# Kernel optimization log

Measured on AMD Instinct MI355X. Metric: run time of the kernel, lower is better.

## Reference

```python
import jax, jax.numpy as jnp
import numpy as np

B, N, D = 256, 512, 64  # batch, positions, channels; units = spatial_units = D


def setup_inputs() -> dict:
    key = jax.random.key(0)
    ks = jax.random.split(key, 9)
    g = 1.0 / np.sqrt(D)  # glorot-ish scale for square matrices
    return {
        "x": jax.random.normal(ks[0], (B, N, D), dtype=jnp.float32),
        "Wq_t": jax.random.normal(ks[1], (D, D), dtype=jnp.float32) * g,
        "Wk_t": jax.random.normal(ks[2], (D, D), dtype=jnp.float32) * g,
        "Wv_t": jax.random.normal(ks[3], (D, D), dtype=jnp.float32) * g,
        "Wq_s": jax.random.normal(ks[4], (D, D), dtype=jnp.float32) * g,
        "Wk_s": jax.random.normal(ks[5], (D, D), dtype=jnp.float32) * g,
        "Wv_s": jax.random.normal(ks[6], (D, D), dtype=jnp.float32) * g,
        "Wd_t": jax.random.normal(ks[7], (D, D), dtype=jnp.float32) * g,
        "bd_t": jnp.zeros((D,), dtype=jnp.float32),
        "Wd_s": jax.random.normal(ks[8], (D, D), dtype=jnp.float32) * g,
        "bd_s": jnp.zeros((D,), dtype=jnp.float32),
    }


def _branch(x, Wq, Wk, Wv, Wd, bd):
    # x: [B, N, D]; one self-attention branch followed by a Dense layer.
    q = jnp.einsum("bnd,de->bne", x, Wq)
    k = jnp.einsum("bnd,de->bne", x, Wk)
    v = jnp.einsum("bnd,de->bne", x, Wv)
    scale = 1.0 / jnp.sqrt(jnp.asarray(Wk.shape[-1], dtype=x.dtype))
    scores = jnp.einsum("bne,bme->bnm", q, k) * scale  # [B, N, N]
    w = jax.nn.softmax(scores, axis=-1)
    attn = jnp.einsum("bnm,bmd->bnd", w, v)
    return jnp.einsum("bnd,de->bne", attn, Wd) + bd


def reference(x, Wq_t, Wk_t, Wv_t, Wq_s, Wk_s, Wv_s, Wd_t, bd_t, Wd_s, bd_s):
    temporal = _branch(x, Wq_t, Wk_t, Wv_t, Wd_t, bd_t)
    spatial = _branch(x, Wq_s, Wk_s, Wv_s, Wd_s, bd_s)
    gate = jax.nn.sigmoid(temporal + spatial)
    return x * gate
```

## Files before the change

kernel.cpp:

```cpp
#include <hip/hip_runtime.h>

typedef __attribute__((ext_vector_type(8))) short short8;
typedef __attribute__((ext_vector_type(4))) short short4v;
typedef __attribute__((ext_vector_type(4))) float float4v;

#define MFMA16(a, b, c) __builtin_amdgcn_mfma_f32_16x16x32_bf16((a), (b), (c), 0, 0, 0)

constexpr int kN = 512;
constexpr int kD = 64;
constexpr int kThreads = 512;

constexpr int LDS_TOTAL_BYTES = 163840;

static __device__ __forceinline__ unsigned short f2bf(float f) {
  unsigned int u = __float_as_uint(f);
  u = (u + 0x7fffu + ((u >> 16) & 1u)) >> 16;
  return (unsigned short)u;
}

__global__ __launch_bounds__(kThreads, 2) void ts_attn_fused(
    const float* __restrict__ x, const float* __restrict__ Wq_t,
    const float* __restrict__ Wk_t, const float* __restrict__ Wv_t,
    const float* __restrict__ Wq_s, const float* __restrict__ Wk_s,
    const float* __restrict__ Wv_s, const float* __restrict__ Wd_t,
    const float* __restrict__ bd_t, const float* __restrict__ Wd_s,
    const float* __restrict__ bd_s, float* __restrict__ out,
    unsigned short* __restrict__ qws) {
  extern __shared__ __align__(16) unsigned short smem_us[];
  unsigned short* Ksw = smem_us;
  unsigned short* Vsw = smem_us + 32768;
  unsigned short* Wdsw = smem_us + 65536;
  unsigned short* Rreg = smem_us + 69632;

  const int tid = threadIdx.x;
  const int wv = tid >> 6;
  const int lane = tid & 63;
  const int ln = lane & 15;
  const int quad = lane >> 4;
  const int b = blockIdx.x;

  const float* xb = x + (size_t)b * (kN * kD);
  float* outb = out + (size_t)b * (kN * kD);
  unsigned short* qb = qws + (size_t)b * (kN * kD);

  float bdsum[4];
#pragma unroll
  for (int nt = 0; nt < 4; ++nt) bdsum[nt] = bd_t[nt * 16 + ln] + bd_s[nt * 16 + ln];

#pragma unroll 1
  for (int br = 0; br < 2; ++br) {
    const float* Wq = br ? Wq_s : Wq_t;
    const float* Wk = br ? Wk_s : Wk_t;
    const float* Wv = br ? Wv_s : Wv_t;
    const float* Wd = br ? Wd_s : Wd_t;

    {
      const int d = tid >> 3;
      const int e0 = (tid & 7) * 8;
      const int base = (d >> 3) * 512 + (d & 7);
      const float* srcs[4] = {Wq, Wk, Wv, Wd};
      unsigned short* dsts[4] = {Rreg, Rreg + 4096, Rreg + 8192, Wdsw};
#pragma unroll
      for (int g = 0; g < 4; ++g) {
        const float4v* p = reinterpret_cast<const float4v*>(srcs[g] + d * 64 + e0);
        const float4v u = p[0];
        const float4v v = p[1];
        unsigned short* dst = dsts[g];
#pragma unroll
        for (int i = 0; i < 4; ++i) dst[base + (e0 + i) * 8] = f2bf(u[i]);
#pragma unroll
        for (int i = 0; i < 4; ++i) dst[base + (e0 + 4 + i) * 8] = f2bf(v[i]);
      }
    }
    __syncthreads();

#pragma unroll 1
    for (int mi = 0; mi < 4; ++mi) {
      const int mt = wv + mi * 8;
      const int mrow = mt * 16 + ln;
      short8 xa0, xa1;
      {
        const float4v* p0 = reinterpret_cast<const float4v*>(xb + mrow * 64 + quad * 8);
        const float4v u0 = p0[0], v0 = p0[1];
        const float4v* p1 = reinterpret_cast<const float4v*>(xb + mrow * 64 + 32 + quad * 8);
        const float4v u1 = p1[0], v1 = p1[1];
#pragma unroll
        for (int i = 0; i < 4; ++i) {
          xa0[i] = (short)f2bf(u0[i]);
          xa0[4 + i] = (short)f2bf(v0[i]);
          xa1[i] = (short)f2bf(u1[i]);
          xa1[4 + i] = (short)f2bf(v1[i]);
        }
      }
#pragma unroll
      for (int g = 0; g < 3; ++g) {
        const unsigned short* Wl = Rreg + g * 4096;
#pragma unroll
        for (int nt = 0; nt < 4; ++nt) {
          const short8 b0 = *reinterpret_cast<const short8*>(Wl + quad * 512 + (nt * 16 + ln) * 8);
          const short8 b1 = *reinterpret_cast<const short8*>(Wl + (4 + quad) * 512 + (nt * 16 + ln) * 8);
          float4v acc = {0.f, 0.f, 0.f, 0.f};
          acc = MFMA16(xa0, b0, acc);
          acc = MFMA16(xa1, b1, acc);
          if (g == 0) {
            const int ehi = nt * 2 + (ln >> 3);
            const int elo = ln & 7;
#pragma unroll
            for (int r = 0; r < 4; ++r)
              qb[ehi * 4096 + (mt * 16 + quad * 4 + r) * 8 + elo] = f2bf(acc[r]);
          } else if (g == 1) {
            const int ehi = nt * 2 + (ln >> 3);
            const int elo = ln & 7;
#pragma unroll
            for (int r = 0; r < 4; ++r)
              Ksw[ehi * 4096 + (mt * 16 + quad * 4 + r) * 8 + elo] = f2bf(acc[r]);
          } else {
            short4v pk;
#pragma unroll
            for (int r = 0; r < 4; ++r) pk[r] = (short)f2bf(acc[r]);
            const int vbase =
                (mt * 2 + (quad >> 1)) * 512 + (nt * 16 + ln) * 8 + (quad & 1) * 4;
            *reinterpret_cast<short4v*>(Vsw + vbase) = pk;
          }
        }
      }
    }
    __syncthreads();

    unsigned short* buf = Rreg + wv * 1152;
#pragma unroll 1
    for (int qi = 0; qi < 4; ++qi) {
      const int qt = wv + qi * 8;
      const short8 q0 = *reinterpret_cast<const short8*>(qb + quad * 4096 + (qt * 16 + ln) * 8);
      const short8 q1 = *reinterpret_cast<const short8*>(qb + (4 + quad) * 4096 + (qt * 16 + ln) * 8);

      float4v s[32];
#pragma unroll
      for (int nt = 0; nt < 32; ++nt) {
        const short8 k0 = *reinterpret_cast<const short8*>(Ksw + quad * 4096 + (nt * 16 + ln) * 8);
        const short8 k1 = *reinterpret_cast<const short8*>(Ksw + (4 + quad) * 4096 + (nt * 16 + ln) * 8);
        float4v acc = {0.f, 0.f, 0.f, 0.f};
        acc = MFMA16(q0, k0, acc);
        acc = MFMA16(q1, k1, acc);
        s[nt] = acc;
      }

      float mx[4] = {-3.0e38f, -3.0e38f, -3.0e38f, -3.0e38f};
#pragma unroll
      for (int nt = 0; nt < 32; ++nt)
#pragma unroll
        for (int r = 0; r < 4; ++r) mx[r] = fmaxf(mx[r], s[nt][r]);
#pragma unroll
      for (int dd = 1; dd < 16; dd <<= 1)
#pragma unroll
        for (int r = 0; r < 4; ++r) mx[r] = fmaxf(mx[r], __shfl_xor(mx[r], dd, 64));

      float sum[4] = {0.f, 0.f, 0.f, 0.f};
      float4v o[4];
#pragma unroll
      for (int i = 0; i < 4; ++i) o[i] = (float4v){0.f, 0.f, 0.f, 0.f};

#pragma unroll
      for (int kc = 0; kc < 16; ++kc) {
#pragma unroll
        for (int t2 = 0; t2 < 2; ++t2) {
          const int nt = kc * 2 + t2;
#pragma unroll
          for (int r = 0; r < 4; ++r) {
            const float p = __expf((s[nt][r] - mx[r]) * 0.125f);
            sum[r] += p;
            buf[(quad * 4 + r) * 72 + t2 * 16 + ln] = f2bf(p);
          }
        }
        asm volatile("s_waitcnt lgkmcnt(0)" ::: "memory");
        const short8 pa = *reinterpret_cast<const short8*>(buf + ln * 72 + quad * 8);
#pragma unroll
        for (int nto = 0; nto < 4; ++nto) {
          const short8 vf =
              *reinterpret_cast<const short8*>(Vsw + (kc * 4 + quad) * 512 + (nto * 16 + ln) * 8);
          o[nto] = MFMA16(pa, vf, o[nto]);
        }
      }

#pragma unroll
      for (int dd = 1; dd < 16; dd <<= 1)
#pragma unroll
        for (int r = 0; r < 4; ++r) sum[r] += __shfl_xor(sum[r], dd, 64);
      float inv[4];
#pragma unroll
      for (int r = 0; r < 4; ++r) inv[r] = 1.0f / sum[r];

#pragma unroll
      for (int nto = 0; nto < 4; ++nto)
#pragma unroll
        for (int r = 0; r < 4; ++r)
          buf[(quad * 4 + r) * 72 + nto * 16 + ln] = f2bf(o[nto][r] * inv[r]);
      asm volatile("s_waitcnt lgkmcnt(0)" ::: "memory");
      const short8 a0 = *reinterpret_cast<const short8*>(buf + ln * 72 + quad * 8);
      const short8 a1 = *reinterpret_cast<const short8*>(buf + ln * 72 + 32 + quad * 8);

#pragma unroll
      for (int nt = 0; nt < 4; ++nt) {
        const short8 w0 = *reinterpret_cast<const short8*>(Wdsw + quad * 512 + (nt * 16 + ln) * 8);
        const short8 w1 = *reinterpret_cast<const short8*>(Wdsw + (4 + quad) * 512 + (nt * 16 + ln) * 8);
        float4v d4 = {0.f, 0.f, 0.f, 0.f};
        d4 = MFMA16(a0, w0, d4);
        d4 = MFMA16(a1, w1, d4);
        const int m0 = qt * 16 + quad * 4;
        const int col = nt * 16 + ln;
        if (br == 0) {
#pragma unroll
          for (int r = 0; r < 4; ++r) outb[(m0 + r) * 64 + col] = d4[r];
        } else {
#pragma unroll
          for (int r = 0; r < 4; ++r) {
            const float z = outb[(m0 + r) * 64 + col] + d4[r] + bdsum[nt];
            const float gate = 1.0f / (1.0f + __expf(-z));
            outb[(m0 + r) * 64 + col] = xb[(m0 + r) * 64 + col] * gate;
          }
        }
      }
    }
    __syncthreads();
  }
}

extern "C" void kernel_launch(void* const* d_in, const int* in_sizes, int n_in,
                              void* d_out, int out_size, void* d_ws, size_t ws_size,
                              hipStream_t stream) {
  const float* x = (const float*)d_in[0];
  const float* Wq_t = (const float*)d_in[1];
  const float* Wk_t = (const float*)d_in[2];
  const float* Wv_t = (const float*)d_in[3];
  const float* Wq_s = (const float*)d_in[4];
  const float* Wk_s = (const float*)d_in[5];
  const float* Wv_s = (const float*)d_in[6];
  const float* Wd_t = (const float*)d_in[7];
  const float* bd_t = (const float*)d_in[8];
  const float* Wd_s = (const float*)d_in[9];
  const float* bd_s = (const float*)d_in[10];
  float* out = (float*)d_out;
  unsigned short* qws = (unsigned short*)d_ws;

  hipFuncSetAttribute(reinterpret_cast<const void*>(ts_attn_fused),
                      hipFuncAttributeMaxDynamicSharedMemorySize, LDS_TOTAL_BYTES);
  ts_attn_fused<<<dim3(256), dim3(kThreads), LDS_TOTAL_BYTES, stream>>>(
      x, Wq_t, Wk_t, Wv_t, Wq_s, Wk_s, Wv_s, Wd_t, bd_t, Wd_s, bd_s, out, qws);
}
```

Before: 193.4 us.

## Stream QK scores without max pass, double threads, keep temporal branch in registers

```diff
diff --git a/kernel.cpp b/kernel.cpp
--- a/kernel.cpp
+++ b/kernel.cpp
@@ -8,9 +8,9 @@
 
 constexpr int kN = 512;
 constexpr int kD = 64;
-constexpr int kThreads = 512;
-
-constexpr int LDS_TOTAL_BYTES = 163840;
+constexpr int kThreads = 1024;
+
+constexpr int LDS_TOTAL_BYTES = 79872 * 2;
 
 static __device__ __forceinline__ unsigned short f2bf(float f) {
   unsigned int u = __float_as_uint(f);
@@ -18,7 +18,7 @@
   return (unsigned short)u;
 }
 
-__global__ __launch_bounds__(kThreads, 2) void ts_attn_fused(
+__global__ __launch_bounds__(kThreads, 4) void ts_attn_fused(
     const float* __restrict__ x, const float* __restrict__ Wq_t,
     const float* __restrict__ Wk_t, const float* __restrict__ Wv_t,
     const float* __restrict__ Wq_s, const float* __restrict__ Wk_s,
@@ -30,7 +30,7 @@
   unsigned short* Ksw = smem_us;
   unsigned short* Vsw = smem_us + 32768;
   unsigned short* Wdsw = smem_us + 65536;
-  unsigned short* Rreg = smem_us + 69632;
+  unsigned short* rep = smem_us + 69632;
 
   const int tid = threadIdx.x;
   const int wv = tid >> 6;
@@ -43,9 +43,15 @@
   float* outb = out + (size_t)b * (kN * kD);
   unsigned short* qb = qws + (size_t)b * (kN * kD);
 
+  const int sd = tid >> 4;
+  const int se0 = (tid & 15) * 4;
+  const int sbase = (sd >> 3) * 512 + (sd & 7);
+
   float bdsum[4];
 #pragma unroll
   for (int nt = 0; nt < 4; ++nt) bdsum[nt] = bd_t[nt * 16 + ln] + bd_s[nt * 16 + ln];
+
+  float4v acc_t[2][4];
 
 #pragma unroll 1
   for (int br = 0; br < 2; ++br) {
@@ -55,28 +61,21 @@
     const float* Wd = br ? Wd_s : Wd_t;
 
     {
-      const int d = tid >> 3;
-      const int e0 = (tid & 7) * 8;
-      const int base = (d >> 3) * 512 + (d & 7);
-      const float* srcs[4] = {Wq, Wk, Wv, Wd};
-      unsigned short* dsts[4] = {Rreg, Rreg + 4096, Rreg + 8192, Wdsw};
-#pragma unroll
-      for (int g = 0; g < 4; ++g) {
-        const float4v* p = reinterpret_cast<const float4v*>(srcs[g] + d * 64 + e0);
-        const float4v u = p[0];
-        const float4v v = p[1];
+      const float* srcs[3] = {Wq, Wk, Wv};
+      unsigned short* dsts[3] = {rep, rep + 4096, Wdsw};
+#pragma unroll
+      for (int g = 0; g < 3; ++g) {
+        const float4v u = *reinterpret_cast<const float4v*>(srcs[g] + sd * 64 + se0);
         unsigned short* dst = dsts[g];
 #pragma unroll
-        for (int i = 0; i < 4; ++i) dst[base + (e0 + i) * 8] = f2bf(u[i]);
-#pragma unroll
-        for (int i = 0; i < 4; ++i) dst[base + (e0 + 4 + i) * 8] = f2bf(v[i]);
+        for (int i = 0; i < 4; ++i) dst[sbase + (se0 + i) * 8] = f2bf(u[i]);
       }
     }
     __syncthreads();
 
 #pragma unroll 1
-    for (int mi = 0; mi < 4; ++mi) {
-      const int mt = wv + mi * 8;
+    for (int mi = 0; mi < 2; ++mi) {
+      const int mt = wv + mi * 16;
       const int mrow = mt * 16 + ln;
       short8 xa0, xa1;
       {
@@ -94,7 +93,7 @@
       }
 #pragma unroll
       for (int g = 0; g < 3; ++g) {
-        const unsigned short* Wl = Rreg + g * 4096;
+        const unsigned short* Wl = (g == 0) ? rep : (g == 1) ? (rep + 4096) : Wdsw;
 #pragma unroll
         for (int nt = 0; nt < 4; ++nt) {
           const short8 b0 = *reinterpret_cast<const short8*>(Wl + quad * 512 + (nt * 16 + ln) * 8);
@@ -127,59 +126,52 @@
     }
     __syncthreads();
 
-    unsigned short* buf = Rreg + wv * 1152;
+    {
+      const float4v u = *reinterpret_cast<const float4v*>(Wd + sd * 64 + se0);
+#pragma unroll
+      for (int i = 0; i < 4; ++i) Wdsw[sbase + (se0 + i) * 8] = f2bf(u[i]);
+    }
+    __syncthreads();
+
+    unsigned short* buf = rep + wv * 640;
 #pragma unroll 1
-    for (int qi = 0; qi < 4; ++qi) {
-      const int qt = wv + qi * 8;
+    for (int qi = 0; qi < 2; ++qi) {
+      const int qt = wv + qi * 16;
       const short8 q0 = *reinterpret_cast<const short8*>(qb + quad * 4096 + (qt * 16 + ln) * 8);
       const short8 q1 = *reinterpret_cast<const short8*>(qb + (4 + quad) * 4096 + (qt * 16 + ln) * 8);
 
-      float4v s[32];
-#pragma unroll
-      for (int nt = 0; nt < 32; ++nt) {
-        const short8 k0 = *reinterpret_cast<const short8*>(Ksw + quad * 4096 + (nt * 16 + ln) * 8);
-        const short8 k1 = *reinterpret_cast<const short8*>(Ksw + (4 + quad) * 4096 + (nt * 16 + ln) * 8);
-        float4v acc = {0.f, 0.f, 0.f, 0.f};
-        acc = MFMA16(q0, k0, acc);
-        acc = MFMA16(q1, k1, acc);
-        s[nt] = acc;
-      }
-
-      float mx[4] = {-3.0e38f, -3.0e38f, -3.0e38f, -3.0e38f};
-#pragma unroll
-      for (int nt = 0; nt < 32; ++nt)
-#pragma unroll
-        for (int r = 0; r < 4; ++r) mx[r] = fmaxf(mx[r], s[nt][r]);
-#pragma unroll
-      for (int dd = 1; dd < 16; dd <<= 1)
-#pragma unroll
-        for (int r = 0; r < 4; ++r) mx[r] = fmaxf(mx[r], __shfl_xor(mx[r], dd, 64));
-
       float sum[4] = {0.f, 0.f, 0.f, 0.f};
       float4v o[4];
 #pragma unroll
       for (int i = 0; i < 4; ++i) o[i] = (float4v){0.f, 0.f, 0.f, 0.f};
 
-#pragma unroll
+#pragma unroll 2
       for (int kc = 0; kc < 16; ++kc) {
 #pragma unroll
         for (int t2 = 0; t2 < 2; ++t2) {
           const int nt = kc * 2 + t2;
+          const short8 k0 = *reinterpret_cast<const short8*>(Ksw + quad * 4096 + (nt * 16 + ln) * 8);
+          const short8 k1 =
+              *reinterpret_cast<const short8*>(Ksw + (4 + quad) * 4096 + (nt * 16 + ln) * 8);
+          float4v acc = {0.f, 0.f, 0.f, 0.f};
+          acc = MFMA16(q0, k0, acc);
+          acc = MFMA16(q1, k1, acc);
 #pragma unroll
           for (int r = 0; r < 4; ++r) {
-            const float p = __expf((s[nt][r] - mx[r]) * 0.125f);
+            const float p = __expf(acc[r] * 0.125f);
             sum[r] += p;
-            buf[(quad * 4 + r) * 72 + t2 * 16 + ln] = f2bf(p);
+            buf[(quad * 4 + r) * 40 + t2 * 16 + ln] = f2bf(p);
           }
         }
         asm volatile("s_waitcnt lgkmcnt(0)" ::: "memory");
-        const short8 pa = *reinterpret_cast<const short8*>(buf + ln * 72 + quad * 8);
+        const short8 pa = *reinterpret_cast<const short8*>(buf + ln * 40 + quad * 8);
 #pragma unroll
         for (int nto = 0; nto < 4; ++nto) {
           const short8 vf =
               *reinterpret_cast<const short8*>(Vsw + (kc * 4 + quad) * 512 + (nto * 16 + ln) * 8);
           o[nto] = MFMA16(pa, vf, o[nto]);
         }
+        asm volatile("s_waitcnt lgkmcnt(0)" ::: "memory");
       }
 
 #pragma unroll
@@ -191,13 +183,20 @@
       for (int r = 0; r < 4; ++r) inv[r] = 1.0f / sum[r];
 
 #pragma unroll
-      for (int nto = 0; nto < 4; ++nto)
+      for (int nto = 0; nto < 2; ++nto)
 #pragma unroll
         for (int r = 0; r < 4; ++r)
-          buf[(quad * 4 + r) * 72 + nto * 16 + ln] = f2bf(o[nto][r] * inv[r]);
+          buf[(quad * 4 + r) * 40 + nto * 16 + ln] = f2bf(o[nto][r] * inv[r]);
       asm volatile("s_waitcnt lgkmcnt(0)" ::: "memory");
-      const short8 a0 = *reinterpret_cast<const short8*>(buf + ln * 72 + quad * 8);
-      const short8 a1 = *reinterpret_cast<const short8*>(buf + ln * 72 + 32 + quad * 8);
+      const short8 a0 = *reinterpret_cast<const short8*>(buf + ln * 40 + quad * 8);
+      asm volatile("s_waitcnt lgkmcnt(0)" ::: "memory");
+#pragma unroll
+      for (int nto = 2; nto < 4; ++nto)
+#pragma unroll
+        for (int r = 0; r < 4; ++r)
+          buf[(quad * 4 + r) * 40 + (nto - 2) * 16 + ln] = f2bf(o[nto][r] * inv[r]);
+      asm volatile("s_waitcnt lgkmcnt(0)" ::: "memory");
+      const short8 a1 = *reinterpret_cast<const short8*>(buf + ln * 40 + quad * 8);
 
 #pragma unroll
       for (int nt = 0; nt < 4; ++nt) {
@@ -206,15 +205,14 @@
         float4v d4 = {0.f, 0.f, 0.f, 0.f};
         d4 = MFMA16(a0, w0, d4);
         d4 = MFMA16(a1, w1, d4);
-        const int m0 = qt * 16 + quad * 4;
-        const int col = nt * 16 + ln;
         if (br == 0) {
-#pragma unroll
-          for (int r = 0; r < 4; ++r) outb[(m0 + r) * 64 + col] = d4[r];
+          acc_t[qi][nt] = d4;
         } else {
+          const int m0 = qt * 16 + quad * 4;
+          const int col = nt * 16 + ln;
 #pragma unroll
           for (int r = 0; r < 4; ++r) {
-            const float z = outb[(m0 + r) * 64 + col] + d4[r] + bdsum[nt];
+            const float z = acc_t[qi][nt][r] + d4[r] + bdsum[nt];
             const float gate = 1.0f / (1.0f + __expf(-z));
             outb[(m0 + r) * 64 + col] = xb[(m0 + r) * 64 + col] * gate;
           }
```

After: 208.7 us. 7.9% more time.
